# Optimization experiments

Measured on AMD Instinct MI355X. Metric: run time of the kernel, lower is better.

Reference implementation:

```python
import jax, jax.numpy as jnp
import numpy as np

B, D, E, H, F, V = 65536, 8, 16, 80, 9, 100000
IN = E * (F + 1)  # 160


def setup_inputs() -> dict:
    key = jax.random.key(0)
    ks = jax.random.split(key, 14)
    pid = jax.random.randint(ks[0], (B,), 0, D + 1)            # 0 = padding, 1..D = domains
    feats = jax.random.randint(ks[1], (B, F), 0, V)
    emb_pid = (jax.random.normal(ks[2], (D + 1, E), jnp.float32) * 0.1).at[0].set(0.0)
    emb_feats = (jax.random.normal(ks[3], (F, V + 1, E), jnp.float32) * 0.1).at[:, 0, :].set(0.0)
    shared_w1 = jax.random.normal(ks[4], (IN, H), jnp.float32) * 0.1
    dom_w1 = jax.random.normal(ks[5], (D, IN, H), jnp.float32) * 0.1
    shared_b1 = jax.random.normal(ks[6], (H,), jnp.float32) * 0.1
    dom_b1 = jax.random.normal(ks[7], (D, H), jnp.float32) * 0.1
    shared_w2 = jax.random.normal(ks[8], (H,), jnp.float32) * 0.1
    dom_w2 = jax.random.normal(ks[9], (D, H), jnp.float32) * 0.1
    shared_b2 = jax.random.normal(ks[10], (), jnp.float32) * 0.1
    dom_b2 = jax.random.normal(ks[11], (D,), jnp.float32) * 0.1
    dl_w = jax.random.normal(ks[12], (E,), jnp.float32) * 0.1
    dl_b = jax.random.normal(ks[13], (), jnp.float32) * 0.1
    return {"pid": pid, "feats": feats, "emb_pid": emb_pid, "emb_feats": emb_feats,
            "shared_w1": shared_w1, "dom_w1": dom_w1, "shared_b1": shared_b1, "dom_b1": dom_b1,
            "shared_w2": shared_w2, "dom_w2": dom_w2, "shared_b2": shared_b2, "dom_b2": dom_b2,
            "dl_w": dl_w, "dl_b": dl_b}


def reference(pid, feats, emb_pid, emb_feats, shared_w1, dom_w1, shared_b1, dom_b1,
              shared_w2, dom_w2, shared_b2, dom_b2, dl_w, dl_b):
    # embedding lookup + relu (dropout is identity at inference)
    e_pid = jax.nn.relu(emb_pid[pid])                          # (B, E)
    e_f = jax.nn.relu(emb_feats[jnp.arange(F), feats])         # (B, F, E)
    out = jnp.concatenate([e_pid, e_f.reshape(B, F * E)], axis=-1)  # (B, IN)
    # star-merge: elementwise product of shared and per-domain kernels, additive biases
    W1 = shared_w1[None] * dom_w1                              # (D, IN, H)
    b1 = shared_b1[None] + dom_b1                              # (D, H)
    h = jax.nn.relu(jnp.einsum('bi,dih->dbh', out, W1) + b1[:, None, :])  # (D, B, H)
    W2 = shared_w2[None] * dom_w2                              # (D, H)
    b2 = shared_b2 + dom_b2                                    # (D,)
    l = jnp.einsum('dbh,dh->db', h, W2) + b2[:, None]          # (D, B)
    # scatter-combine: each sample takes its own domain's logit (0 for padding pid)
    sel = pid[None, :] == (jnp.arange(D) + 1)[:, None]         # (D, B)
    logits = jnp.sum(jnp.where(sel, l, 0.0), axis=0)           # (B,)
    domain_logits = e_pid @ dl_w + dl_b                        # (B,)
    return logits + domain_logits
```

## Files before the change

kernel.cpp:

```cpp
#include <hip/hip_runtime.h>

#define NB 65536
#define ND 8
#define NE 16
#define NH 80
#define NF 9
#define NV 100000
#define NIN 160
#define WND 512

typedef __attribute__((ext_vector_type(8))) short short8;
typedef __attribute__((ext_vector_type(4))) float float4v;

#define WS_W1BF   0
#define WS_B1F    51200
#define WS_W2F    51840
#define WS_B2F    52480

__device__ inline unsigned short f2bf(float x) {
  unsigned int u = __float_as_uint(x);
  return (unsigned short)((u + 0x7fffu + ((u >> 16) & 1u)) >> 16);
}

__global__ void k_fuse(const float* __restrict__ sw1, const float* __restrict__ dw1,
                       const float* __restrict__ sb1, const float* __restrict__ db1,
                       const float* __restrict__ sw2, const float* __restrict__ dw2,
                       const float* __restrict__ sb2, const float* __restrict__ db2,
                       unsigned int* __restrict__ w1bf, float* __restrict__ wsf) {
  int t = blockIdx.x * 256 + threadIdx.x;
  if (t < ND * NH * (NIN / 2)) {
    int d = t / (NH * (NIN / 2));
    int r = t % (NH * (NIN / 2));
    int n = r / (NIN / 2);
    int k0 = (r % (NIN / 2)) * 2;
    float a = sw1[k0 * NH + n] * dw1[d * NIN * NH + k0 * NH + n];
    float b = sw1[(k0 + 1) * NH + n] * dw1[d * NIN * NH + (k0 + 1) * NH + n];
    w1bf[t] = (unsigned)f2bf(a) | ((unsigned)f2bf(b) << 16);
  }
  if (t < ND * NH) {
    wsf[WS_B1F + t] = sb1[t % NH] + db1[t];
    wsf[WS_W2F + t] = sw2[t % NH] * dw2[t];
  }
  if (t < ND) wsf[WS_B2F + t] = sb2[0] + db2[t];
}

__global__ __launch_bounds__(256) void k_main(
    const int* __restrict__ pid, const int* __restrict__ feats,
    const float* __restrict__ emb_pid, const float* __restrict__ emb_feats,
    const float* __restrict__ dl_w, const float* __restrict__ dl_b,
    const unsigned int* __restrict__ w1bf, const float* __restrict__ wsf,
    float* __restrict__ out) {
  const int d = blockIdx.x & 7;
  const int wnd = blockIdx.x >> 3;
  const int t = threadIdx.x, wave = t >> 6, lane = t & 63;

  __shared__ unsigned short sA[64][168];
  __shared__ unsigned short sB[80][168];
  __shared__ int sid[WND];
  __shared__ int cnt[2][4];

  const int b0 = wnd * WND + t;
  const int b1 = b0 + 256;
  const int p0 = pid[b0];
  const int p1 = pid[b1];

  const unsigned int* __restrict__ wb = w1bf + d * (NH * (NIN / 2));
  for (int i = t; i < NH * (NIN / 2); i += 256) {
    int n = i / (NIN / 2), kp = i % (NIN / 2);
    ((unsigned int*)&sB[n][0])[kp] = wb[i];
  }

  const float dlb = dl_b[0];
  if (d == 0) {
    if (p0 == 0) out[b0] = dlb;
    if (p1 == 0) out[b1] = dlb;
  }

  unsigned long long m0 = __ballot(p0 == d + 1);
  unsigned long long m1 = __ballot(p1 == d + 1);
  if (lane == 0) { cnt[0][wave] = (int)__popcll(m0); cnt[1][wave] = (int)__popcll(m1); }
  const int r0 = (int)__popcll(m0 & ((1ull << lane) - 1ull));
  const int r1 = (int)__popcll(m1 & ((1ull << lane) - 1ull));

  float dlacc = dlb;
  unsigned int ep[8];
  {
    const float* __restrict__ row = emb_pid + (d + 1) * NE;
#pragma unroll
    for (int i = 0; i < NE; i += 2) {
      float x0 = fmaxf(row[i], 0.f), x1 = fmaxf(row[i + 1], 0.f);
      dlacc = fmaf(x0, dl_w[i], dlacc);
      dlacc = fmaf(x1, dl_w[i + 1], dlacc);
      ep[i >> 1] = (unsigned)f2bf(x0) | ((unsigned)f2bf(x1) << 16);
    }
  }
  const float b2 = wsf[WS_B2F + d];
  float b1l[5], w2l[5];
#pragma unroll
  for (int nt = 0; nt < 5; ++nt) {
    b1l[nt] = wsf[WS_B1F + d * NH + nt * 16 + (lane & 15)];
    w2l[nt] = wsf[WS_W2F + d * NH + nt * 16 + (lane & 15)];
  }

  __syncthreads();
  int base0 = 0, base1 = 0;
#pragma unroll
  for (int w = 0; w < 4; ++w) {
    if (w < wave) { base0 += cnt[0][w]; base1 += cnt[1][w]; }
  }
  const int tot0 = cnt[0][0] + cnt[0][1] + cnt[0][2] + cnt[0][3];
  const int c = tot0 + cnt[1][0] + cnt[1][1] + cnt[1][2] + cnt[1][3];
  if (p0 == d + 1) sid[base0 + r0] = b0;
  if (p1 == d + 1) sid[tot0 + base1 + r1] = b1;
  __syncthreads();

  for (int g0 = 0; g0 < c; g0 += 64) {
    const int s = t >> 2, q = t & 3;
    const int ss = g0 + s;
    const int bb = sid[ss < c ? ss : 0];
    int idx[NF];
#pragma unroll
    for (int f = 0; f < NF; ++f) idx[f] = feats[bb * NF + f];
    float4 vv[NF];
#pragma unroll
    for (int f = 0; f < NF; ++f)
      vv[f] = ((const float4*)(emb_feats + ((size_t)f * (NV + 1) + (size_t)idx[f]) * NE))[q];
    if (q < 2) {
      unsigned int* dst = (unsigned int*)&sA[s][0];
#pragma unroll
      for (int j = 0; j < 4; ++j) dst[q * 4 + j] = ep[q * 4 + j];
    }
#pragma unroll
    for (int f = 0; f < NF; ++f) {
      unsigned int pk0 = (unsigned)f2bf(fmaxf(vv[f].x, 0.f)) |
                         ((unsigned)f2bf(fmaxf(vv[f].y, 0.f)) << 16);
      unsigned int pk1 = (unsigned)f2bf(fmaxf(vv[f].z, 0.f)) |
                         ((unsigned)f2bf(fmaxf(vv[f].w, 0.f)) << 16);
      unsigned int* dst = (unsigned int*)&sA[s][16 + f * 16];
      dst[q * 2] = pk0;
      dst[q * 2 + 1] = pk1;
    }
    __syncthreads();

    float4v acc[5];
#pragma unroll
    for (int nt = 0; nt < 5; ++nt)
      acc[nt] = (float4v){b1l[nt], b1l[nt], b1l[nt], b1l[nt]};
    const int arow = wave * 16 + (lane & 15);
    const int koff = (lane >> 4) * 8;
#pragma unroll
    for (int ks = 0; ks < 5; ++ks) {
      short8 af = *(const short8*)&sA[arow][ks * 32 + koff];
#pragma unroll
      for (int nt = 0; nt < 5; ++nt) {
        short8 bf = *(const short8*)&sB[nt * 16 + (lane & 15)][ks * 32 + koff];
        acc[nt] = __builtin_amdgcn_mfma_f32_16x16x32_bf16(af, bf, acc[nt], 0, 0, 0);
      }
    }

    float pr[4];
#pragma unroll
    for (int r = 0; r < 4; ++r) {
      float a2 = 0.f;
#pragma unroll
      for (int nt = 0; nt < 5; ++nt) a2 = fmaf(fmaxf(acc[nt][r], 0.f), w2l[nt], a2);
      pr[r] = a2;
    }
#pragma unroll
    for (int r = 0; r < 4; ++r) {
      pr[r] += __shfl_xor(pr[r], 1);
      pr[r] += __shfl_xor(pr[r], 2);
      pr[r] += __shfl_xor(pr[r], 4);
      pr[r] += __shfl_xor(pr[r], 8);
    }
    if ((lane & 15) == 0) {
      int srow = wave * 16 + (lane >> 4) * 4;
#pragma unroll
      for (int r = 0; r < 4; ++r) {
        int kk = g0 + srow + r;
        if (kk < c) out[sid[kk]] = pr[r] + b2 + dlacc;
      }
    }
    __syncthreads();
  }
}

extern "C" void kernel_launch(void* const* d_in, const int* in_sizes, int n_in,
                              void* d_out, int out_size, void* d_ws, size_t ws_size,
                              hipStream_t stream) {
  const int*   pid      = (const int*)d_in[0];
  const int*   feats    = (const int*)d_in[1];
  const float* emb_pid  = (const float*)d_in[2];
  const float* emb_f    = (const float*)d_in[3];
  const float* sw1      = (const float*)d_in[4];
  const float* dw1      = (const float*)d_in[5];
  const float* sb1      = (const float*)d_in[6];
  const float* db1      = (const float*)d_in[7];
  const float* sw2      = (const float*)d_in[8];
  const float* dw2      = (const float*)d_in[9];
  const float* sb2      = (const float*)d_in[10];
  const float* db2      = (const float*)d_in[11];
  const float* dl_w     = (const float*)d_in[12];
  const float* dl_b     = (const float*)d_in[13];
  float* out = (float*)d_out;
  float* wsf = (float*)d_ws;
  unsigned int* w1bf = (unsigned int*)d_ws;

  k_fuse<<<(ND * NH * (NIN / 2) + 255) / 256, 256, 0, stream>>>(
      sw1, dw1, sb1, db1, sw2, dw2, sb2, db2, w1bf, wsf);
  k_main<<<(NB / WND) * ND, 256, 0, stream>>>(pid, feats, emb_pid, emb_f,
                                              dl_w, dl_b, w1bf, wsf, out);
}
```

Measured before the change: 29.75 us.

## Build MFMA A fragments directly in registers, dropping shared-memory staging

```diff
diff --git a/kernel.cpp b/kernel.cpp
--- a/kernel.cpp
+++ b/kernel.cpp
@@ -1,4 +1,5 @@
 #include <hip/hip_runtime.h>
+#include <hip/hip_bf16.h>
 
 #define NB 65536
 #define ND 8
@@ -17,9 +18,10 @@
 #define WS_W2F    51840
 #define WS_B2F    52480
 
-__device__ inline unsigned short f2bf(float x) {
-  unsigned int u = __float_as_uint(x);
-  return (unsigned short)((u + 0x7fffu + ((u >> 16) & 1u)) >> 16);
+__device__ inline unsigned int cvt2(float x, float y) {
+  union { __hip_bfloat162 h; unsigned int u; } cv;
+  cv.h = __float22bfloat162_rn(make_float2(x, y));
+  return cv.u;
 }
 
 __global__ void k_fuse(const float* __restrict__ sw1, const float* __restrict__ dw1,
@@ -35,7 +37,7 @@
     int k0 = (r % (NIN / 2)) * 2;
     float a = sw1[k0 * NH + n] * dw1[d * NIN * NH + k0 * NH + n];
     float b = sw1[(k0 + 1) * NH + n] * dw1[d * NIN * NH + (k0 + 1) * NH + n];
-    w1bf[t] = (unsigned)f2bf(a) | ((unsigned)f2bf(b) << 16);
+    w1bf[t] = cvt2(a, b);
   }
   if (t < ND * NH) {
     wsf[WS_B1F + t] = sb1[t % NH] + db1[t];
@@ -44,7 +46,7 @@
   if (t < ND) wsf[WS_B2F + t] = sb2[0] + db2[t];
 }
 
-__global__ __launch_bounds__(256) void k_main(
+__global__ __launch_bounds__(256, 4) void k_main(
     const int* __restrict__ pid, const int* __restrict__ feats,
     const float* __restrict__ emb_pid, const float* __restrict__ emb_feats,
     const float* __restrict__ dl_w, const float* __restrict__ dl_b,
@@ -54,7 +56,6 @@
   const int wnd = blockIdx.x >> 3;
   const int t = threadIdx.x, wave = t >> 6, lane = t & 63;
 
-  __shared__ unsigned short sA[64][168];
   __shared__ unsigned short sB[80][168];
   __shared__ int sid[WND];
   __shared__ int cnt[2][4];
@@ -64,10 +65,12 @@
   const int p0 = pid[b0];
   const int p1 = pid[b1];
 
-  const unsigned int* __restrict__ wb = w1bf + d * (NH * (NIN / 2));
-  for (int i = t; i < NH * (NIN / 2); i += 256) {
-    int n = i / (NIN / 2), kp = i % (NIN / 2);
-    ((unsigned int*)&sB[n][0])[kp] = wb[i];
+  {
+    const uint4* __restrict__ wb4 = (const uint4*)(w1bf + d * (NH * (NIN / 2)));
+    for (int i = t; i < NH * (NIN / 8); i += 256) {
+      int n = i / 20, c8 = i % 20;
+      *(uint4*)&sB[n][c8 * 8] = wb4[i];
+    }
   }
 
   const float dlb = dl_b[0];
@@ -91,7 +94,7 @@
       float x0 = fmaxf(row[i], 0.f), x1 = fmaxf(row[i + 1], 0.f);
       dlacc = fmaf(x0, dl_w[i], dlacc);
       dlacc = fmaf(x1, dl_w[i + 1], dlacc);
-      ep[i >> 1] = (unsigned)f2bf(x0) | ((unsigned)f2bf(x1) << 16);
+      ep[i >> 1] = cvt2(x0, x1);
     }
   }
   const float b2 = wsf[WS_B2F + d];
@@ -105,56 +108,70 @@
   __syncthreads();
   int base0 = 0, base1 = 0;
 #pragma unroll
-  for (int w = 0; w < 4; ++w) {
+  for (int w = 0; w < 4; ++w)
     if (w < wave) { base0 += cnt[0][w]; base1 += cnt[1][w]; }
-  }
   const int tot0 = cnt[0][0] + cnt[0][1] + cnt[0][2] + cnt[0][3];
   const int c = tot0 + cnt[1][0] + cnt[1][1] + cnt[1][2] + cnt[1][3];
   if (p0 == d + 1) sid[base0 + r0] = b0;
   if (p1 == d + 1) sid[tot0 + base1 + r1] = b1;
   __syncthreads();
 
+  const int q = lane >> 4;
+  const int koff = q * 8;
+
   for (int g0 = 0; g0 < c; g0 += 64) {
-    const int s = t >> 2, q = t & 3;
-    const int ss = g0 + s;
-    const int bb = sid[ss < c ? ss : 0];
-    int idx[NF];
-#pragma unroll
-    for (int f = 0; f < NF; ++f) idx[f] = feats[bb * NF + f];
-    float4 vv[NF];
-#pragma unroll
-    for (int f = 0; f < NF; ++f)
-      vv[f] = ((const float4*)(emb_feats + ((size_t)f * (NV + 1) + (size_t)idx[f]) * NE))[q];
-    if (q < 2) {
-      unsigned int* dst = (unsigned int*)&sA[s][0];
-#pragma unroll
-      for (int j = 0; j < 4; ++j) dst[q * 4 + j] = ep[q * 4 + j];
-    }
-#pragma unroll
-    for (int f = 0; f < NF; ++f) {
-      unsigned int pk0 = (unsigned)f2bf(fmaxf(vv[f].x, 0.f)) |
-                         ((unsigned)f2bf(fmaxf(vv[f].y, 0.f)) << 16);
-      unsigned int pk1 = (unsigned)f2bf(fmaxf(vv[f].z, 0.f)) |
-                         ((unsigned)f2bf(fmaxf(vv[f].w, 0.f)) << 16);
-      unsigned int* dst = (unsigned int*)&sA[s][16 + f * 16];
-      dst[q * 2] = pk0;
-      dst[q * 2 + 1] = pk1;
-    }
-    __syncthreads();
+    const int srow = g0 + wave * 16 + (lane & 15);
+    const int bb = sid[srow < c ? srow : 0];
+
+    int off[5];
+#pragma unroll
+    for (int ks = 0; ks < 5; ++ks) {
+      int m = q + 4 * ks;
+      if (m >= 2) {
+        int f = (m - 2) >> 1;
+        off[ks] = (f * (NV + 1) + feats[bb * NF + f]) * NE + ((m - 2) & 1) * 8;
+      }
+    }
+    float4 lo[5], hi[5];
+#pragma unroll
+    for (int ks = 0; ks < 5; ++ks) {
+      int m = q + 4 * ks;
+      if (m >= 2) {
+        const float4* __restrict__ src = (const float4*)(emb_feats + (size_t)off[ks]);
+        lo[ks] = src[0];
+        hi[ks] = src[1];
+      }
+    }
+    unsigned int e0 = q ? ep[4] : ep[0];
+    unsigned int e1 = q ? ep[5] : ep[1];
+    unsigned int e2 = q ? ep[6] : ep[2];
+    unsigned int e3 = q ? ep[7] : ep[3];
+    short8 af[5];
+#pragma unroll
+    for (int ks = 0; ks < 5; ++ks) {
+      int m = q + 4 * ks;
+      union { unsigned int u[4]; short8 s; } cv;
+      if (m < 2) {
+        cv.u[0] = e0; cv.u[1] = e1; cv.u[2] = e2; cv.u[3] = e3;
+      } else {
+        cv.u[0] = cvt2(fmaxf(lo[ks].x, 0.f), fmaxf(lo[ks].y, 0.f));
+        cv.u[1] = cvt2(fmaxf(lo[ks].z, 0.f), fmaxf(lo[ks].w, 0.f));
+        cv.u[2] = cvt2(fmaxf(hi[ks].x, 0.f), fmaxf(hi[ks].y, 0.f));
+        cv.u[3] = cvt2(fmaxf(hi[ks].z, 0.f), fmaxf(hi[ks].w, 0.f));
+      }
+      af[ks] = cv.s;
+    }
 
     float4v acc[5];
 #pragma unroll
     for (int nt = 0; nt < 5; ++nt)
       acc[nt] = (float4v){b1l[nt], b1l[nt], b1l[nt], b1l[nt]};
-    const int arow = wave * 16 + (lane & 15);
-    const int koff = (lane >> 4) * 8;
-#pragma unroll
-    for (int ks = 0; ks < 5; ++ks) {
-      short8 af = *(const short8*)&sA[arow][ks * 32 + koff];
+#pragma unroll
+    for (int ks = 0; ks < 5; ++ks) {
 #pragma unroll
       for (int nt = 0; nt < 5; ++nt) {
         short8 bf = *(const short8*)&sB[nt * 16 + (lane & 15)][ks * 32 + koff];
-        acc[nt] = __builtin_amdgcn_mfma_f32_16x16x32_bf16(af, bf, acc[nt], 0, 0, 0);
+        acc[nt] = __builtin_amdgcn_mfma_f32_16x16x32_bf16(af[ks], bf, acc[nt], 0, 0, 0);
       }
     }
 
@@ -174,14 +191,13 @@
       pr[r] += __shfl_xor(pr[r], 8);
     }
     if ((lane & 15) == 0) {
-      int srow = wave * 16 + (lane >> 4) * 4;
+      int srow2 = wave * 16 + (lane >> 4) * 4;
 #pragma unroll
       for (int r = 0; r < 4; ++r) {
-        int kk = g0 + srow + r;
+        int kk = g0 + srow2 + r;
         if (kk < c) out[sid[kk]] = pr[r] + b2 + dlacc;
       }
     }
-    __syncthreads();
   }
 }
 
```

New measurement: 52.87 us. +77.7%, slower.
